# Kernel tuning notes

Measured on AMD Instinct MI355X. Metric: run time of the kernel, lower is better.

Reference implementation:

```python
import jax, jax.numpy as jnp
import numpy as np

N = 384          # residues / nodes
E = 12288        # edges (avg degree 32)
D_LM = 1024      # BERT hidden
D_NODE = 256     # extra node features -> D_LM + D_NODE = 1280
D = 1280         # node_emb_size
H = D // 10      # 128, dis/mask MLP hidden
M = 64           # masked positions


def setup_inputs() -> dict:
    key = jax.random.key(0)
    ks = jax.random.split(key, 16)
    s = lambda d_in: 1.0 / np.sqrt(d_in)
    inp = {
        "lm_embedding": jax.random.normal(ks[0], (1, N + 2, D_LM), jnp.float32),
        "node_feat": jax.random.normal(ks[1], (N, D_NODE), jnp.float32),
        # positive distances in [0.5, 1.5) so edge_weight = 1/(d^2+1e-6) is well scaled
        "edge_feat": jax.random.uniform(ks[2], (E, 1), jnp.float32) + 0.5,
        "src": jax.random.randint(ks[3], (E,), 0, N, jnp.int32),
        "dst": jax.random.randint(ks[4], (E,), 0, N, jnp.int32),
        "mask_index": jax.random.randint(ks[5], (M,), 0, N, jnp.int32),
        # GINConv apply-func linears (stored as [in, out]; torch Linear is x @ W.T + b)
        "W_gin0": jax.random.normal(ks[6], (D, D), jnp.float32) * s(D),
        "b_gin0": jnp.zeros((D,), jnp.float32),
        "W_gin1": jax.random.normal(ks[7], (D, D), jnp.float32) * s(D),
        "b_gin1": jnp.zeros((D,), jnp.float32),
        # dis_nn: Linear(D,H) -> ReLU -> Linear(H,30)
        "Wd1": jax.random.normal(ks[8], (D, H), jnp.float32) * s(D),
        "bd1": jnp.zeros((H,), jnp.float32),
        "Wd2": jax.random.normal(ks[9], (H, 30), jnp.float32) * s(H),
        "bd2": jnp.zeros((30,), jnp.float32),
        # mask_nn: Linear(D,H) -> ReLU -> Linear(H,2) -> Tanh
        "Wm1": jax.random.normal(ks[10], (D, H), jnp.float32) * s(D),
        "bm1": jnp.zeros((H,), jnp.float32),
        "Wm2": jax.random.normal(ks[11], (H, 2), jnp.float32) * s(H),
        "bm2": jnp.zeros((2,), jnp.float32),
    }
    return inp


def _gin(x, src, dst, edge_weight, W, b):
    # DGL GINConv (eps=0, 'sum'): Linear( x + sum_{e:(u->v)} w_e * x_u )
    msg = x[src] * edge_weight                      # [E, D] gather-multiply
    agg = jax.ops.segment_sum(msg, dst, num_segments=N)  # scatter-sum to dst
    return (x + agg) @ W + b


def reference(lm_embedding, node_feat, edge_feat, src, dst, mask_index,
              W_gin0, b_gin0, W_gin1, b_gin1,
              Wd1, bd1, Wd2, bd2, Wm1, bm1, Wm2, bm2):
    # node_feat0: strip CLS/SEP tokens, concat with node features -> [N, D]
    node_feat0 = jnp.concatenate([lm_embedding[0, 1:-1, :], node_feat], axis=1)
    edge_weight = 1.0 / (edge_feat ** 2 + 1e-6)     # [E, 1]

    # original uses node_feat0.data (detached) as GIN input
    x0 = jax.lax.stop_gradient(node_feat0)
    h = _gin(x0, src, dst, edge_weight, W_gin0, b_gin0)
    node_output = _gin(h, src, dst, edge_weight, W_gin1, b_gin1)
    node_output = node_output + node_feat0          # residual (use_lm=1)

    # pairwise squared differences: [N, N, D]
    dis_hid = (node_output[None, :, :] - node_output[:, None, :]) ** 2
    dh = dis_hid.reshape(-1, D)                     # [N*N, D]
    dis_pred = jax.nn.relu(dh @ Wd1 + bd1) @ Wd2 + bd2  # [N*N, 30]

    xm = node_output[mask_index]                    # [M, D]
    mask_pred = jnp.tanh(jax.nn.relu(xm @ Wm1 + bm1) @ Wm2 + bm2)  # [M, 2]
    return dis_pred, mask_pred
```

## Files before the change

### kernel.cpp

```cpp
#include <hip/hip_runtime.h>
#include <hip/hip_bf16.h>

#define NN 384
#define EE 12288
#define DD 1280
#define HH 128
#define DISROWS (NN*NN)

typedef short bf16x8 __attribute__((ext_vector_type(8)));
typedef short bf16x4 __attribute__((ext_vector_type(4)));
typedef float f32x4  __attribute__((ext_vector_type(4)));

__device__ __forceinline__ unsigned short f2bf(float x){
  unsigned u = __builtin_bit_cast(unsigned, x);
  u += 0x7fffu + ((u >> 16) & 1u);
  return (unsigned short)(u >> 16);
}
__device__ __forceinline__ float bf2f(unsigned short h){
  unsigned u = ((unsigned)h) << 16;
  return __builtin_bit_cast(float, u);
}
__device__ __forceinline__ short f2bf_fast(float x){
  return (short)__bfloat16_as_ushort(__float2bfloat16(x));
}
__device__ __forceinline__ void glds16(const short* g, short* l){
  __builtin_amdgcn_global_load_lds((const __attribute__((address_space(1))) void*)g,
                                   (__attribute__((address_space(3))) void*)l, 16, 0, 0);
}

__device__ __forceinline__ void tsplit_body(const float* __restrict__ W,
                                            short* __restrict__ Thi, short* __restrict__ Tlo,
                                            int R, int C, int bx, int by, int t,
                                            float* tile ){
  int rb = by*64, cb = bx*64;
  int r  = t >> 2;
  int cs = (t & 3) * 16;
  const float* sp = W + (long)(rb + r)*C + cb + cs;
  #pragma unroll
  for (int i = 0; i < 16; i += 4){
    f32x4 v = *(const f32x4*)(sp + i);
    tile[r*65 + cs+i+0] = v[0]; tile[r*65 + cs+i+1] = v[1];
    tile[r*65 + cs+i+2] = v[2]; tile[r*65 + cs+i+3] = v[3];
  }
  __syncthreads();
  int cp = t >> 2;
  int rs = (t & 3) * 16;
  bf16x8 vh0, vh1, vl0, vl1;
  #pragma unroll
  for (int i = 0; i < 8; ++i){
    float f = tile[(rs+i)*65 + cp];
    unsigned short h = f2bf(f);
    vh0[i] = (short)h; vl0[i] = (short)f2bf(f - bf2f(h));
  }
  #pragma unroll
  for (int i = 0; i < 8; ++i){
    float f = tile[(rs+8+i)*65 + cp];
    unsigned short h = f2bf(f);
    vh1[i] = (short)h; vl1[i] = (short)f2bf(f - bf2f(h));
  }
  long ob = (long)(cb + cp)*R + rb + rs;
  *(bf16x8*)&Thi[ob]   = vh0;
  *(bf16x8*)&Thi[ob+8] = vh1;
  if (Tlo){
    *(bf16x8*)&Tlo[ob]   = vl0;
    *(bf16x8*)&Tlo[ob+8] = vl1;
  }
}

__global__ void k_prep(const float* __restrict__ lm, const float* __restrict__ nf,
                       float* __restrict__ x0,
                       const int* __restrict__ dst, const float* __restrict__ ef,
                       int* __restrict__ offs, int* __restrict__ sorted,
                       float* __restrict__ ew,
                       const float* __restrict__ Wd1, short* __restrict__ W1t,
                       const float* __restrict__ Wd2, short* __restrict__ W2t,
                       const float* __restrict__ Wg0, short* __restrict__ WtAh,
                       short* __restrict__ WtAl){
  __shared__ __align__(16) float sh[64*65];
  const int b = blockIdx.x;
  const int t = threadIdx.x;
  if (b < 960){
    int i = b*512 + t;
    int n = i / 1280;
    int d = i - n*1280;
    x0[i] = (d < 1024) ? lm[(n+1)*1024 + d] : nf[n*256 + (d-1024)];
    return;
  }
  if (b == 960){
    int* cnt = (int*)sh;
    int* base = cnt + 512;
    if (t < 512) cnt[t] = 0;
    __syncthreads();
    for (int e = t; e < EE; e += 512){
      atomicAdd(&cnt[dst[e]], 1);
      float f = ef[e];
      ew[e] = 1.0f/(f*f + 1e-6f);
    }
    __syncthreads();
    for (int off = 1; off < 512; off <<= 1){
      int v = (t >= off) ? cnt[t - off] : 0;
      __syncthreads();
      cnt[t] += v;
      __syncthreads();
    }
    if (t < NN){
      int excl = t ? cnt[t-1] : 0;
      offs[t] = excl;
      base[t] = excl;
    }
    if (t == 0) offs[NN] = EE;
    __syncthreads();
    for (int e = t; e < EE; e += 512){
      int p = atomicAdd(&base[dst[e]], 1);
      sorted[p] = e;
    }
    return;
  }
  if (b < 1002){
    int g = b - 961;
    if (g < 40){
      if (t < 256) tsplit_body(Wd1, W1t, nullptr, DD, HH, g & 1, g >> 1, t, sh);
      else { __syncthreads(); }
      return;
    }
    for (int i = t; i < 32*HH; i += 512){
      int c = i >> 7, h = i & 127;
      float v = (c < 30) ? Wd2[h*30 + c] : 0.f;
      W2t[i] = (short)f2bf(v);
    }
    return;
  }
  {
    int g = b - 1002;
    if (t < 256) tsplit_body(Wg0, WtAh, WtAl, DD, DD, g % 20, g / 20, t, sh);
    else { __syncthreads(); }
  }
}

__global__ void k_agg(const float* __restrict__ X, const float* __restrict__ ew,
                      const int* __restrict__ src, const int* __restrict__ offs,
                      const int* __restrict__ sorted, float* __restrict__ Y){
  __shared__ int   s_off[160];
  __shared__ float s_w[160];
  const int v = blockIdx.x;
  const int d = blockIdx.y*256 + threadIdx.x;
  const int t = threadIdx.x;
  float acc = X[(long)v*DD + d];
  const int b = offs[v], e = offs[v+1];
  for (int c0 = b; c0 < e; c0 += 160){
    int n = e - c0; if (n > 160) n = 160;
    __syncthreads();
    if (t < n){
      int eid = sorted[c0 + t];
      s_off[t] = src[eid]*DD;
      s_w[t]   = ew[eid];
    }
    __syncthreads();
    int k = 0;
    for (; k + 4 <= n; k += 4){
      acc += s_w[k]  *X[s_off[k]   + d];
      acc += s_w[k+1]*X[s_off[k+1] + d];
      acc += s_w[k+2]*X[s_off[k+2] + d];
      acc += s_w[k+3]*X[s_off[k+3] + d];
    }
    for (; k < n; ++k) acc += s_w[k]*X[s_off[k] + d];
  }
  Y[(long)v*DD + d] = acc;
}

__launch_bounds__(256, 2)
__global__ void k_gin_gemm(const float* __restrict__ Y, const short* __restrict__ Whi,
                           const short* __restrict__ Wlo, float* __restrict__ P){
  __shared__ __align__(16) short Ahi[128*40], Alo[128*40], Bhi[128*40], Blo[128*40];
  const int m0 = blockIdx.x*128;
  const int n0 = blockIdx.y*128;
  const int kbase = blockIdx.z*320;
  const int t = threadIdx.x, w = t >> 6, lane = t & 63;
  const int l15 = lane & 15, l4 = lane >> 4;
  f32x4 acc[2][8];
  #pragma unroll
  for (int m = 0; m < 2; ++m)
    #pragma unroll
    for (int n = 0; n < 8; ++n) acc[m][n] = (f32x4){0.f,0.f,0.f,0.f};

  const int row = t >> 1, half = t & 1;
  const float* ap  = Y   + (long)(m0+row)*DD + half*16;
  const short* bph = Whi + (long)(n0+row)*DD + half*16;
  const short* bpl = Wlo + (long)(n0+row)*DD + half*16;

  for (int kk = 0; kk < 10; ++kk){
    int d0 = kbase + kk*32;
    __syncthreads();
    #pragma unroll
    for (int g = 0; g < 2; ++g){
      f32x4 v0 = *(const f32x4*)(ap + d0 + g*8);
      f32x4 v1 = *(const f32x4*)(ap + d0 + g*8 + 4);
      bf16x8 vh, vl;
      #pragma unroll
      for (int q = 0; q < 4; ++q){
        unsigned short h0 = f2bf(v0[q]);
        vh[q]   = (short)h0; vl[q]   = (short)f2bf(v0[q] - bf2f(h0));
        unsigned short h1 = f2bf(v1[q]);
        vh[4+q] = (short)h1; vl[4+q] = (short)f2bf(v1[q] - bf2f(h1));
      }
      *(bf16x8*)&Ahi[row*40 + half*16 + g*8] = vh;
      *(bf16x8*)&Alo[row*40 + half*16 + g*8] = vl;
    }
    *(bf16x8*)&Bhi[row*40 + half*16]     = *(const bf16x8*)(bph + d0);
    *(bf16x8*)&Bhi[row*40 + half*16 + 8] = *(const bf16x8*)(bph + d0 + 8);
    *(bf16x8*)&Blo[row*40 + half*16]     = *(const bf16x8*)(bpl + d0);
    *(bf16x8*)&Blo[row*40 + half*16 + 8] = *(const bf16x8*)(bpl + d0 + 8);
    __syncthreads();

    bf16x8 ah[2], al[2];
    #pragma unroll
    for (int m = 0; m < 2; ++m){
      int rr = w*32 + m*16 + l15;
      ah[m] = *(const bf16x8*)&Ahi[rr*40 + l4*8];
      al[m] = *(const bf16x8*)&Alo[rr*40 + l4*8];
    }
    #pragma unroll
    for (int n = 0; n < 8; ++n){
      int rr = n*16 + l15;
      bf16x8 bh = *(const bf16x8*)&Bhi[rr*40 + l4*8];
      bf16x8 bl = *(const bf16x8*)&Blo[rr*40 + l4*8];
      #pragma unroll
      for (int m = 0; m < 2; ++m){
        acc[m][n] = __builtin_amdgcn_mfma_f32_16x16x32_bf16(ah[m], bh, acc[m][n], 0,0,0);
        acc[m][n] = __builtin_amdgcn_mfma_f32_16x16x32_bf16(ah[m], bl, acc[m][n], 0,0,0);
        acc[m][n] = __builtin_amdgcn_mfma_f32_16x16x32_bf16(al[m], bh, acc[m][n], 0,0,0);
      }
    }
  }
  float* Pz = P + (long)blockIdx.z*NN*DD;
  #pragma unroll
  for (int m = 0; m < 2; ++m){
    #pragma unroll
    for (int n = 0; n < 8; ++n){
      int gr0 = m0 + w*32 + m*16 + l4*4;
      int gc  = n0 + n*16 + l15;
      #pragma unroll
      for (int r = 0; r < 4; ++r)
        Pz[(long)(gr0+r)*DD + gc] = acc[m][n][r];
    }
  }
}

__global__ void k_red_t(const float* __restrict__ P, const float* __restrict__ bias,
                        const float* __restrict__ resid, float* __restrict__ Out,
                        const float* __restrict__ Wg1, short* __restrict__ WtAh,
                        short* __restrict__ WtAl){
  __shared__ __align__(16) float sh[64*65];
  const int b = blockIdx.x;
  if (b >= 480){
    if (Wg1){
      int g = b - 480;
      tsplit_body(Wg1, WtAh, WtAl, DD, DD, g % 20, g / 20, threadIdx.x, sh);
    }
    return;
  }
  const int i = b*256 + threadIdx.x;
  const int col = (i*4) % DD;
  const f32x4* P4 = (const f32x4*)P;
  f32x4 s = P4[i];
  s += P4[i + 122880];
  s += P4[i + 2*122880];
  s += P4[i + 3*122880];
  s += *(const f32x4*)(bias + col);
  if (resid) s += ((const f32x4*)resid)[i];
  ((f32x4*)Out)[i] = s;
}

__launch_bounds__(256, 3)
__global__ void k_dis(const float* __restrict__ X, const short* __restrict__ W1t,
                      const float* __restrict__ bd1, const short* __restrict__ W2t,
                      const float* __restrict__ bd2, float* __restrict__ out,
                      const int* __restrict__ midx,
                      const float* __restrict__ Wm1, const float* __restrict__ bm1,
                      const float* __restrict__ Wm2, const float* __restrict__ bm2){
  __shared__ __align__(16) short smem[25088];
  const int b = blockIdx.x;
  const int t = threadIdx.x;

  if (b >= 600){
    float* tl = (float*)smem;
    int m = b - 600;
    if (t < HH){
      const float* x = X + (long)midx[m]*DD;
      float a0 = 0.f, a1 = 0.f, a2 = 0.f, a3 = 0.f;
      for (int d = 0; d < DD; d += 4){
        a0 += x[d]   * Wm1[(d)*HH + t];
        a1 += x[d+1] * Wm1[(d+1)*HH + t];
        a2 += x[d+2] * Wm1[(d+2)*HH + t];
        a3 += x[d+3] * Wm1[(d+3)*HH + t];
      }
      float v = a0 + a1 + a2 + a3 + bm1[t];
      tl[t] = v > 0.f ? v : 0.f;
    }
    __syncthreads();
    if (t < 2){
      float s = bm2[t];
      for (int h = 0; h < HH; ++h) s += tl[h]*Wm2[h*2 + t];
      out[(long)DISROWS*30 + m*2 + t] = tanhf(s);
    }
    return;
  }

  int k = 0, rem = b;
  while (rem >= 2*(24 - k)){ rem -= 2*(24 - k); ++k; }
  int ib = 2*k;
  if (rem >= 24 - k){ ++ib; rem -= 24 - k; }
  const int jb = k + rem;
  const int i0 = ib*8, j0 = jb*16;

  const int w = t >> 6, lane = t & 63;
  const int l15 = lane & 15, l4 = lane >> 4;

  short* WA = smem;
  float* XF = (float*)(smem + 16384);
  short* TL = smem;
  float* OT = (float*)(smem + 17408);

  f32x4 acc[2][8];
  #pragma unroll
  for (int m = 0; m < 2; ++m)
    #pragma unroll
    for (int n = 0; n < 8; ++n) acc[m][n] = (f32x4){0.f,0.f,0.f,0.f};

  const short* wsrc[4];
  #pragma unroll
  for (int i = 0; i < 4; ++i){
    int hb = w*32 + i*8 + (lane >> 3);
    wsrc[i] = W1t + (long)hb*DD + (((lane & 7) ^ (hb & 7))*8);
  }
  const float* xsrc[6];
  int xli[6];
  #pragma unroll
  for (int g = 0; g < 6; ++g){
    int idx = g*256 + t;
    int rowl = idx >> 6, col = idx & 63;
    int grow = (rowl < 8) ? (i0 + rowl) : (j0 + rowl - 8);
    xsrc[g] = X + (long)grow*DD + col;
    xli[g] = rowl*68 + col;
  }

  float xr[6];
  #pragma unroll
  for (int i = 0; i < 4; ++i)
    glds16(wsrc[i], WA + (w*32 + i*8)*64);
  #pragma unroll
  for (int g = 0; g < 6; ++g) xr[g] = xsrc[g][0];
  #pragma unroll
  for (int g = 0; g < 6; ++g) XF[xli[g]] = xr[g];
  __syncthreads();

  for (int mk = 0; mk < 20; ++mk){
    const int cb = mk & 1;
    short* WAc = WA + cb*8192;
    float* XFc = XF + cb*1632;
    short* WAn = WA + (cb^1)*8192;
    float* XFn = XF + (cb^1)*1632;
    if (mk < 19){
      #pragma unroll
      for (int i = 0; i < 4; ++i)
        glds16(wsrc[i] + (mk+1)*64, WAn + (w*32 + i*8)*64);
      #pragma unroll
      for (int g = 0; g < 6; ++g) xr[g] = xsrc[g][(mk+1)*64];
    }
    #pragma unroll
    for (int ks = 0; ks < 2; ++ks){
      f32x4 xj0 = *(const f32x4*)&XFc[(8 + l15)*68 + ks*32 + l4*8];
      f32x4 xj1 = *(const f32x4*)&XFc[(8 + l15)*68 + ks*32 + l4*8 + 4];
      bf16x8 a[2];
      #pragma unroll
      for (int m = 0; m < 2; ++m){
        const float* xip = &XFc[(2*w + m)*68 + ks*32 + l4*8];
        f32x4 xi0 = *(const f32x4*)xip;
        f32x4 xi1 = *(const f32x4*)(xip + 4);
        bf16x8 av;
        #pragma unroll
        for (int q = 0; q < 4; ++q){ float dl = xj0[q]-xi0[q]; av[q]   = f2bf_fast(dl*dl); }
        #pragma unroll
        for (int q = 0; q < 4; ++q){ float dl = xj1[q]-xi1[q]; av[4+q] = f2bf_fast(dl*dl); }
        a[m] = av;
      }
      #pragma unroll
      for (int n = 0; n < 8; ++n){
        bf16x8 wf = *(const bf16x8*)&WAc[(n*16 + l15)*64 + (((ks*4 + l4) ^ (l15 & 7))*8)];
        acc[0][n] = __builtin_amdgcn_mfma_f32_16x16x32_bf16(wf, a[0], acc[0][n], 0,0,0);
        acc[1][n] = __builtin_amdgcn_mfma_f32_16x16x32_bf16(wf, a[1], acc[1][n], 0,0,0);
      }
    }
    if (mk < 19){
      #pragma unroll
      for (int g = 0; g < 6; ++g) XFn[xli[g]] = xr[g];
    }
    __syncthreads();
  }

  f32x4 bd1v[8];
  #pragma unroll
  for (int n = 0; n < 8; ++n) bd1v[n] = *(const f32x4*)(bd1 + n*16 + l4*4);
  #pragma unroll
  for (int m = 0; m < 2; ++m){
    int pair = (2*w + m)*16 + l15;
    #pragma unroll
    for (int n = 0; n < 8; ++n){
      bf16x4 pv;
      #pragma unroll
      for (int r = 0; r < 4; ++r){
        float v = acc[m][n][r] + bd1v[n][r];
        v = v > 0.f ? v : 0.f;
        pv[r] = f2bf_fast(v);
      }
      *(bf16x4*)&TL[pair*136 + n*16 + l4*4] = pv;
    }
  }
  __syncthreads();

  f32x4 acc2[2][2];
  #pragma unroll
  for (int m2 = 0; m2 < 2; ++m2)
    #pragma unroll
    for (int nn = 0; nn < 2; ++nn) acc2[m2][nn] = (f32x4){0.f,0.f,0.f,0.f};
  #pragma unroll
  for (int hs = 0; hs < 4; ++hs){
    bf16x8 b2[2];
    #pragma unroll
    for (int nn = 0; nn < 2; ++nn)
      b2[nn] = *(const bf16x8*)&W2t[(nn*16 + l15)*HH + hs*32 + l4*8];
    #pragma unroll
    for (int m2 = 0; m2 < 2; ++m2){
      bf16x8 a2 = *(const bf16x8*)&TL[(w*32 + m2*16 + l15)*136 + hs*32 + l4*8];
      #pragma unroll
      for (int nn = 0; nn < 2; ++nn)
        acc2[m2][nn] = __builtin_amdgcn_mfma_f32_16x16x32_bf16(a2, b2[nn], acc2[m2][nn], 0,0,0);
    }
  }
  #pragma unroll
  for (int m2 = 0; m2 < 2; ++m2){
    #pragma unroll
    for (int nn = 0; nn < 2; ++nn){
      int cc = nn*16 + l15;
      if (cc < 30){
        float b2v = bd2[cc];
        #pragma unroll
        for (int r = 0; r < 4; ++r)
          OT[(w*32 + m2*16 + l4*4 + r)*30 + cc] = acc2[m2][nn][r] + b2v;
      }
    }
  }
  __syncthreads();

  {
    int i = t >> 5;
    int ca = (t & 31)*15;
    long nbase = ((long)(i0 + i)*NN + j0)*30 + ca;
    const float* nsrc = OT + i*480 + ca;
    #pragma unroll
    for (int q = 0; q < 15; ++q) out[nbase + q] = nsrc[q];
    int j = t >> 4;
    int s = t & 15;
    int ii = s >> 1;
    int c0 = (s & 1)*15;
    long mbase = ((long)(j0 + j)*NN + i0 + ii)*30 + c0;
    const float* msrc = OT + ii*480 + j*30 + c0;
    #pragma unroll
    for (int q = 0; q < 15; ++q) out[mbase + q] = msrc[q];
  }
}

extern "C" void kernel_launch(void* const* d_in, const int* in_sizes, int n_in,
                              void* d_out, int out_size, void* d_ws, size_t ws_size,
                              hipStream_t stream){
  const float* lm   = (const float*)d_in[0];
  const float* nf   = (const float*)d_in[1];
  const float* ef   = (const float*)d_in[2];
  const int*   src  = (const int*)d_in[3];
  const int*   dst  = (const int*)d_in[4];
  const int*   midx = (const int*)d_in[5];
  const float* Wg0  = (const float*)d_in[6];
  const float* bg0  = (const float*)d_in[7];
  const float* Wg1  = (const float*)d_in[8];
  const float* bg1  = (const float*)d_in[9];
  const float* Wd1  = (const float*)d_in[10];
  const float* bd1  = (const float*)d_in[11];
  const float* Wd2  = (const float*)d_in[12];
  const float* bd2  = (const float*)d_in[13];
  const float* Wm1  = (const float*)d_in[14];
  const float* bm1  = (const float*)d_in[15];
  const float* Wm2  = (const float*)d_in[16];
  const float* bm2  = (const float*)d_in[17];
  float* dis = (float*)d_out;

  char* ws = (char*)d_ws;
  size_t off = 0;
  auto alloc = [&](size_t bytes)->void*{
    void* p = ws + off; off += (bytes + 255) & ~(size_t)255; return p;
  };
  float* x0   = (float*)alloc((size_t)NN*DD*4);
  float* yb   = (float*)alloc((size_t)NN*DD*4);
  float* hb   = (float*)alloc((size_t)NN*DD*4);
  float* ew   = (float*)alloc((size_t)EE*4);
  int*   offs = (int*)alloc((NN+1)*4);
  int*   sorted = (int*)alloc(EE*4);
  short* WtAh = (short*)alloc((size_t)DD*DD*2);
  short* WtAl = (short*)alloc((size_t)DD*DD*2);
  short* W1t  = (short*)alloc((size_t)HH*DD*2);
  short* W2t  = (short*)alloc((size_t)32*HH*2);
  float* P    = (float*)alloc((size_t)4*NN*DD*4);

  k_prep<<<1402,512,0,stream>>>(lm, nf, x0, dst, ef, offs, sorted, ew,
                                Wd1, W1t, Wd2, W2t, Wg0, WtAh, WtAl);

  k_agg<<<dim3(384,5),256,0,stream>>>(x0, ew, src, offs, sorted, yb);
  k_gin_gemm<<<dim3(3,10,4),256,0,stream>>>(yb, WtAh, WtAl, P);
  k_red_t<<<880,256,0,stream>>>(P, bg0, nullptr, hb, Wg1, WtAh, WtAl);

  k_agg<<<dim3(384,5),256,0,stream>>>(hb, ew, src, offs, sorted, yb);
  k_gin_gemm<<<dim3(3,10,4),256,0,stream>>>(yb, WtAh, WtAl, P);
  k_red_t<<<480,256,0,stream>>>(P, bg1, x0, hb, nullptr, nullptr, nullptr);

  k_dis<<<664,256,0,stream>>>(hb, W1t, bd1, W2t, bd2, dis,
                              midx, Wm1, bm1, Wm2, bm2);
}
```

Before: 142.3 us.

## Retile dis-MLP GEMM into 4x4 warp tiles with register-held xi rows

The pairwise-difference GEMM loop is restructured. Each warp now covers 4 i-rows by 64 hidden units instead of 2 i-rows by all 128, and the K step drops from 64 to 32, giving 40 iterations. The xi rows are loaded directly from global memory into registers and only the xj rows are staged in LDS, which shrinks shared memory use and LDS reads per MFMA. In exchange there are twice as many barriers, more per-thread global loads, and higher register pressure from the 4x4 accumulator tile.

New measurement: 159.7 us. +12.2%, slower.

```diff
diff --git a/kernel.cpp b/kernel.cpp
--- a/kernel.cpp
+++ b/kernel.cpp
@@ -10,6 +10,7 @@
 typedef short bf16x8 __attribute__((ext_vector_type(8)));
 typedef short bf16x4 __attribute__((ext_vector_type(4)));
 typedef float f32x4  __attribute__((ext_vector_type(4)));
+typedef float f32x2  __attribute__((ext_vector_type(2)));
 
 __device__ __forceinline__ unsigned short f2bf(float x){
   unsigned u = __builtin_bit_cast(unsigned, x);
@@ -315,97 +316,94 @@
 
   const int w = t >> 6, lane = t & 63;
   const int l15 = lane & 15, l4 = lane >> 4;
+  const int wi = w & 1, wh = w >> 1;
 
   short* WA = smem;
-  float* XF = (float*)(smem + 16384);
+  float* XJ = (float*)(smem + 8192);
   short* TL = smem;
   float* OT = (float*)(smem + 17408);
 
-  f32x4 acc[2][8];
-  #pragma unroll
-  for (int m = 0; m < 2; ++m)
-    #pragma unroll
-    for (int n = 0; n < 8; ++n) acc[m][n] = (f32x4){0.f,0.f,0.f,0.f};
-
-  const short* wsrc[4];
-  #pragma unroll
-  for (int i = 0; i < 4; ++i){
-    int hb = w*32 + i*8 + (lane >> 3);
-    wsrc[i] = W1t + (long)hb*DD + (((lane & 7) ^ (hb & 7))*8);
-  }
-  const float* xsrc[6];
-  int xli[6];
-  #pragma unroll
-  for (int g = 0; g < 6; ++g){
-    int idx = g*256 + t;
-    int rowl = idx >> 6, col = idx & 63;
-    int grow = (rowl < 8) ? (i0 + rowl) : (j0 + rowl - 8);
-    xsrc[g] = X + (long)grow*DD + col;
-    xli[g] = rowl*68 + col;
-  }
-
-  float xr[6];
-  #pragma unroll
-  for (int i = 0; i < 4; ++i)
-    glds16(wsrc[i], WA + (w*32 + i*8)*64);
-  #pragma unroll
-  for (int g = 0; g < 6; ++g) xr[g] = xsrc[g][0];
-  #pragma unroll
-  for (int g = 0; g < 6; ++g) XF[xli[g]] = xr[g];
+  f32x4 acc[4][4];
+  #pragma unroll
+  for (int m = 0; m < 4; ++m)
+    #pragma unroll
+    for (int n = 0; n < 4; ++n) acc[m][n] = (f32x4){0.f,0.f,0.f,0.f};
+
+  const short* wsrc[2]; int wdst[2];
+  #pragma unroll
+  for (int i = 0; i < 2; ++i){
+    int h = (w*2 + i)*16 + (lane >> 2);
+    int s = lane & 3;
+    wsrc[i] = W1t + (long)h*DD + ((s ^ ((h >> 1) & 3))*8);
+    wdst[i] = (w*2 + i)*512;
+  }
+  const float* xjsrc = X + (long)(j0 + (t >> 4))*DD + (t & 15)*2;
+  const int xjli = (t >> 4)*36 + (t & 15)*2;
+  const float* xip[4];
+  #pragma unroll
+  for (int m = 0; m < 4; ++m)
+    xip[m] = X + (long)(i0 + wi*4 + m)*DD + l4*8;
+
+  glds16(wsrc[0], WA + wdst[0]);
+  glds16(wsrc[1], WA + wdst[1]);
+  { f32x2 v = *(const f32x2*)xjsrc; *(f32x2*)&XJ[xjli] = v; }
+  f32x4 xa[4], xb[4];
+  #pragma unroll
+  for (int m = 0; m < 4; ++m){
+    xa[m] = *(const f32x4*)xip[m];
+    xb[m] = *(const f32x4*)(xip[m] + 4);
+  }
   __syncthreads();
 
-  for (int mk = 0; mk < 20; ++mk){
-    const int cb = mk & 1;
-    short* WAc = WA + cb*8192;
-    float* XFc = XF + cb*1632;
-    short* WAn = WA + (cb^1)*8192;
-    float* XFn = XF + (cb^1)*1632;
-    if (mk < 19){
-      #pragma unroll
-      for (int i = 0; i < 4; ++i)
-        glds16(wsrc[i] + (mk+1)*64, WAn + (w*32 + i*8)*64);
-      #pragma unroll
-      for (int g = 0; g < 6; ++g) xr[g] = xsrc[g][(mk+1)*64];
-    }
-    #pragma unroll
-    for (int ks = 0; ks < 2; ++ks){
-      f32x4 xj0 = *(const f32x4*)&XFc[(8 + l15)*68 + ks*32 + l4*8];
-      f32x4 xj1 = *(const f32x4*)&XFc[(8 + l15)*68 + ks*32 + l4*8 + 4];
-      bf16x8 a[2];
-      #pragma unroll
-      for (int m = 0; m < 2; ++m){
-        const float* xip = &XFc[(2*w + m)*68 + ks*32 + l4*8];
-        f32x4 xi0 = *(const f32x4*)xip;
-        f32x4 xi1 = *(const f32x4*)(xip + 4);
-        bf16x8 av;
-        #pragma unroll
-        for (int q = 0; q < 4; ++q){ float dl = xj0[q]-xi0[q]; av[q]   = f2bf_fast(dl*dl); }
-        #pragma unroll
-        for (int q = 0; q < 4; ++q){ float dl = xj1[q]-xi1[q]; av[4+q] = f2bf_fast(dl*dl); }
-        a[m] = av;
+  const int wro = (l4 ^ ((l15 >> 1) & 3))*8;
+  for (int mk = 0; mk < 40; ++mk){
+    const int cur = mk & 1, nxt = cur ^ 1;
+    const int d1 = (mk+1)*32;
+    if (mk < 39){
+      glds16(wsrc[0] + d1, WA + nxt*4096 + wdst[0]);
+      glds16(wsrc[1] + d1, WA + nxt*4096 + wdst[1]);
+    }
+    const float* XJc = XJ + cur*576;
+    f32x4 xj0 = *(const f32x4*)&XJc[l15*36 + l4*8];
+    f32x4 xj1 = *(const f32x4*)&XJc[l15*36 + l4*8 + 4];
+    bf16x8 a[4];
+    #pragma unroll
+    for (int m = 0; m < 4; ++m){
+      bf16x8 av;
+      #pragma unroll
+      for (int q = 0; q < 4; ++q){ float d = xj0[q]-xa[m][q]; av[q]   = f2bf_fast(d*d); }
+      #pragma unroll
+      for (int q = 0; q < 4; ++q){ float d = xj1[q]-xb[m][q]; av[4+q] = f2bf_fast(d*d); }
+      a[m] = av;
+    }
+    if (mk < 39){
+      #pragma unroll
+      for (int m = 0; m < 4; ++m){
+        xa[m] = *(const f32x4*)(xip[m] + d1);
+        xb[m] = *(const f32x4*)(xip[m] + d1 + 4);
       }
-      #pragma unroll
-      for (int n = 0; n < 8; ++n){
-        bf16x8 wf = *(const bf16x8*)&WAc[(n*16 + l15)*64 + (((ks*4 + l4) ^ (l15 & 7))*8)];
-        acc[0][n] = __builtin_amdgcn_mfma_f32_16x16x32_bf16(wf, a[0], acc[0][n], 0,0,0);
-        acc[1][n] = __builtin_amdgcn_mfma_f32_16x16x32_bf16(wf, a[1], acc[1][n], 0,0,0);
-      }
-    }
-    if (mk < 19){
-      #pragma unroll
-      for (int g = 0; g < 6; ++g) XFn[xli[g]] = xr[g];
-    }
-    __syncthreads();
-  }
-
-  f32x4 bd1v[8];
-  #pragma unroll
-  for (int n = 0; n < 8; ++n) bd1v[n] = *(const f32x4*)(bd1 + n*16 + l4*4);
-  #pragma unroll
-  for (int m = 0; m < 2; ++m){
-    int pair = (2*w + m)*16 + l15;
-    #pragma unroll
-    for (int n = 0; n < 8; ++n){
+      f32x2 xjn = *(const f32x2*)(xjsrc + d1);
+      *(f32x2*)&XJ[nxt*576 + xjli] = xjn;
+    }
+    const short* WAc = WA + cur*4096;
+    #pragma unroll
+    for (int n = 0; n < 4; ++n){
+      bf16x8 wf = *(const bf16x8*)&WAc[((wh*4 + n)*16 + l15)*32 + wro];
+      #pragma unroll
+      for (int m = 0; m < 4; ++m)
+        acc[m][n] = __builtin_amdgcn_mfma_f32_16x16x32_bf16(wf, a[m], acc[m][n], 0,0,0);
+    }
+    __syncthreads();
+  }
+
+  f32x4 bd1v[4];
+  #pragma unroll
+  for (int n = 0; n < 4; ++n) bd1v[n] = *(const f32x4*)(bd1 + wh*64 + n*16 + l4*4);
+  #pragma unroll
+  for (int m = 0; m < 4; ++m){
+    int pair = (wi*4 + m)*16 + l15;
+    #pragma unroll
+    for (int n = 0; n < 4; ++n){
       bf16x4 pv;
       #pragma unroll
       for (int r = 0; r < 4; ++r){
@@ -413,7 +411,7 @@
         v = v > 0.f ? v : 0.f;
         pv[r] = f2bf_fast(v);
       }
-      *(bf16x4*)&TL[pair*136 + n*16 + l4*4] = pv;
+      *(bf16x4*)&TL[pair*136 + wh*64 + n*16 + l4*4] = pv;
     }
   }
   __syncthreads();
```

## Fuse GIN prep, aggregation, GEMM and reduce into one persistent kernel with grid barriers

Applied to the files above, without the earlier changes.

Replaces the seven launches for prep, two aggregations, two split-bf16 GEMMs and two reductions with a single persistent 256-block kernel whose stages are separated by a software grid barrier. The edge sort becomes a global atomic count, a scan in block 0 and a parallel placement step. Both GIN weight matrices are now split and transposed up front into separate buffers. GEMM tiles shrink to 128x64 with one 16-row slab per wave. The aim is to remove launch gaps and tail effects between small stages. In exchange it adds barrier spin cost, relies on all 256 blocks being co-resident, and may lose per-stage parallelism.

New measurement: 336.7 us. +136.6%, slower.

```diff
diff --git a/kernel.cpp b/kernel.cpp
--- a/kernel.cpp
+++ b/kernel.cpp
@@ -28,247 +28,257 @@
                                    (__attribute__((address_space(3))) void*)l, 16, 0, 0);
 }
 
-__device__ __forceinline__ void tsplit_body(const float* __restrict__ W,
-                                            short* __restrict__ Thi, short* __restrict__ Tlo,
-                                            int R, int C, int bx, int by, int t,
-                                            float* tile ){
+__device__ __forceinline__ void gridbar(int* ibar){
+  __syncthreads();
+  if (threadIdx.x == 0){
+    __threadfence();
+    int g = atomicAdd(&ibar[1], 0);
+    int v = atomicAdd(&ibar[0], 1);
+    if (v == 255){
+      atomicExch(&ibar[0], 0);
+      atomicAdd(&ibar[1], 1);
+    } else {
+      int iters = 0;
+      while (atomicAdd(&ibar[1], 0) == g && iters < (1<<20)){
+        ++iters;
+        __builtin_amdgcn_s_sleep(8);
+      }
+    }
+    __threadfence();
+  }
+  __syncthreads();
+}
+
+__device__ __forceinline__ void tsplit512(const float* __restrict__ W,
+                                          short* __restrict__ Thi, short* __restrict__ Tlo,
+                                          int R, int C, int bx, int by, int t, float* tile){
   int rb = by*64, cb = bx*64;
-  int r  = t >> 2;
-  int cs = (t & 3) * 16;
+  int r = t >> 3, cs = (t & 7)*8;
   const float* sp = W + (long)(rb + r)*C + cb + cs;
-  #pragma unroll
-  for (int i = 0; i < 16; i += 4){
-    f32x4 v = *(const f32x4*)(sp + i);
-    tile[r*65 + cs+i+0] = v[0]; tile[r*65 + cs+i+1] = v[1];
-    tile[r*65 + cs+i+2] = v[2]; tile[r*65 + cs+i+3] = v[3];
-  }
+  f32x4 v0 = *(const f32x4*)sp;
+  f32x4 v1 = *(const f32x4*)(sp + 4);
+  tile[r*65 + cs+0] = v0[0]; tile[r*65 + cs+1] = v0[1];
+  tile[r*65 + cs+2] = v0[2]; tile[r*65 + cs+3] = v0[3];
+  tile[r*65 + cs+4] = v1[0]; tile[r*65 + cs+5] = v1[1];
+  tile[r*65 + cs+6] = v1[2]; tile[r*65 + cs+7] = v1[3];
   __syncthreads();
-  int cp = t >> 2;
-  int rs = (t & 3) * 16;
-  bf16x8 vh0, vh1, vl0, vl1;
+  int cp = t >> 3, rs = (t & 7)*8;
+  bf16x8 vh, vl;
   #pragma unroll
   for (int i = 0; i < 8; ++i){
     float f = tile[(rs+i)*65 + cp];
     unsigned short h = f2bf(f);
-    vh0[i] = (short)h; vl0[i] = (short)f2bf(f - bf2f(h));
-  }
-  #pragma unroll
-  for (int i = 0; i < 8; ++i){
-    float f = tile[(rs+8+i)*65 + cp];
-    unsigned short h = f2bf(f);
-    vh1[i] = (short)h; vl1[i] = (short)f2bf(f - bf2f(h));
+    vh[i] = (short)h; vl[i] = (short)f2bf(f - bf2f(h));
   }
   long ob = (long)(cb + cp)*R + rb + rs;
-  *(bf16x8*)&Thi[ob]   = vh0;
-  *(bf16x8*)&Thi[ob+8] = vh1;
-  if (Tlo){
-    *(bf16x8*)&Tlo[ob]   = vl0;
-    *(bf16x8*)&Tlo[ob+8] = vl1;
-  }
-}
-
-__global__ void k_prep(const float* __restrict__ lm, const float* __restrict__ nf,
-                       float* __restrict__ x0,
-                       const int* __restrict__ dst, const float* __restrict__ ef,
-                       int* __restrict__ offs, int* __restrict__ sorted,
-                       float* __restrict__ ew,
-                       const float* __restrict__ Wd1, short* __restrict__ W1t,
-                       const float* __restrict__ Wd2, short* __restrict__ W2t,
-                       const float* __restrict__ Wg0, short* __restrict__ WtAh,
-                       short* __restrict__ WtAl){
-  __shared__ __align__(16) float sh[64*65];
-  const int b = blockIdx.x;
-  const int t = threadIdx.x;
-  if (b < 960){
-    int i = b*512 + t;
-    int n = i / 1280;
-    int d = i - n*1280;
-    x0[i] = (d < 1024) ? lm[(n+1)*1024 + d] : nf[n*256 + (d-1024)];
-    return;
-  }
-  if (b == 960){
-    int* cnt = (int*)sh;
-    int* base = cnt + 512;
-    if (t < 512) cnt[t] = 0;
+  *(bf16x8*)&Thi[ob] = vh;
+  if (Tlo) *(bf16x8*)&Tlo[ob] = vl;
+}
+
+__device__ void agg_stage(const float* __restrict__ X, float* __restrict__ Y,
+                          const float* __restrict__ ew, const int* __restrict__ src_,
+                          const int* __restrict__ offs, const int* __restrict__ sorted,
+                          int b, int t, char* sm){
+  int*   s_off = (int*)sm;
+  float* s_w   = (float*)(sm + 2048);
+  for (int u = b; u < 768; u += 256){
+    int v = u >> 1;
+    int dh = (u & 1)*640;
+    int d0 = dh + t;
+    int d1 = dh + 512 + t;
+    float a0 = X[(long)v*DD + d0];
+    float a1 = (t < 128) ? X[(long)v*DD + d1] : 0.f;
+    const int eb = offs[v], ee = offs[v+1];
+    for (int c0 = eb; c0 < ee; c0 += 512){
+      int n = ee - c0; if (n > 512) n = 512;
+      __syncthreads();
+      if (t < n){
+        int eid = sorted[c0 + t];
+        s_off[t] = src_[eid]*DD;
+        s_w[t]   = ew[eid];
+      }
+      __syncthreads();
+      int k = 0;
+      for (; k + 4 <= n; k += 4){
+        a0 += s_w[k]*X[s_off[k]+d0];   a0 += s_w[k+1]*X[s_off[k+1]+d0];
+        a0 += s_w[k+2]*X[s_off[k+2]+d0]; a0 += s_w[k+3]*X[s_off[k+3]+d0];
+        if (t < 128){
+          a1 += s_w[k]*X[s_off[k]+d1];   a1 += s_w[k+1]*X[s_off[k+1]+d1];
+          a1 += s_w[k+2]*X[s_off[k+2]+d1]; a1 += s_w[k+3]*X[s_off[k+3]+d1];
+        }
+      }
+      for (; k < n; ++k){
+        a0 += s_w[k]*X[s_off[k]+d0];
+        if (t < 128) a1 += s_w[k]*X[s_off[k]+d1];
+      }
+    }
+    Y[(long)v*DD + d0] = a0;
+    if (t < 128) Y[(long)v*DD + d1] = a1;
     __syncthreads();
-    for (int e = t; e < EE; e += 512){
-      atomicAdd(&cnt[dst[e]], 1);
-      float f = ef[e];
-      ew[e] = 1.0f/(f*f + 1e-6f);
-    }
+  }
+}
+
+__device__ void gemm_stage(const float* __restrict__ Y, const short* __restrict__ Whi,
+                           const short* __restrict__ Wlo, float* __restrict__ P,
+                           int b, int t, char* sm){
+  if (b < 240){
+    short* Ahi = (short*)sm;
+    short* Alo = Ahi + 5120;
+    short* Bhi = Alo + 5120;
+    short* Blo = Bhi + 2560;
+    const int z = b / 60, rest = b % 60;
+    const int m0 = (rest % 3)*128, n0 = (rest / 3)*64;
+    const int kbase = z*320;
+    const int w = t >> 6, lane = t & 63, l15 = lane & 15, l4 = lane >> 4;
+    f32x4 acc[4];
+    #pragma unroll
+    for (int n = 0; n < 4; ++n) acc[n] = (f32x4){0.f,0.f,0.f,0.f};
+    const int arow = t >> 2, aq = t & 3;
+    const float* ap = Y + (long)(m0 + arow)*DD + aq*8;
+    for (int kk = 0; kk < 10; ++kk){
+      const int d0 = kbase + kk*32;
+      __syncthreads();
+      {
+        f32x4 v0 = *(const f32x4*)(ap + d0);
+        f32x4 v1 = *(const f32x4*)(ap + d0 + 4);
+        bf16x8 vh, vl;
+        #pragma unroll
+        for (int q = 0; q < 4; ++q){
+          unsigned short h0 = f2bf(v0[q]);
+          vh[q]   = (short)h0; vl[q]   = (short)f2bf(v0[q] - bf2f(h0));
+          unsigned short h1 = f2bf(v1[q]);
+          vh[4+q] = (short)h1; vl[4+q] = (short)f2bf(v1[q] - bf2f(h1));
+        }
+        *(bf16x8*)&Ahi[arow*40 + aq*8] = vh;
+        *(bf16x8*)&Alo[arow*40 + aq*8] = vl;
+      }
+      if (t < 256){
+        const short* bph = Whi + (long)(n0 + (t>>2))*DD + (t&3)*8 + d0;
+        const short* bpl = Wlo + (long)(n0 + (t>>2))*DD + (t&3)*8 + d0;
+        *(bf16x8*)&Bhi[(t>>2)*40 + (t&3)*8] = *(const bf16x8*)bph;
+        *(bf16x8*)&Blo[(t>>2)*40 + (t&3)*8] = *(const bf16x8*)bpl;
+      }
+      __syncthreads();
+      bf16x8 ah = *(const bf16x8*)&Ahi[(w*16 + l15)*40 + l4*8];
+      bf16x8 al = *(const bf16x8*)&Alo[(w*16 + l15)*40 + l4*8];
+      #pragma unroll
+      for (int n = 0; n < 4; ++n){
+        bf16x8 bh = *(const bf16x8*)&Bhi[(n*16 + l15)*40 + l4*8];
+        bf16x8 bl = *(const bf16x8*)&Blo[(n*16 + l15)*40 + l4*8];
+        acc[n] = __builtin_amdgcn_mfma_f32_16x16x32_bf16(ah, bh, acc[n], 0,0,0);
+        acc[n] = __builtin_amdgcn_mfma_f32_16x16x32_bf16(ah, bl, acc[n], 0,0,0);
+        acc[n] = __builtin_amdgcn_mfma_f32_16x16x32_bf16(al, bh, acc[n], 0,0,0);
+      }
+    }
+    float* Pz = P + (long)z*NN*DD;
+    #pragma unroll
+    for (int n = 0; n < 4; ++n){
+      int gc = n0 + n*16 + l15;
+      #pragma unroll
+      for (int r = 0; r < 4; ++r)
+        Pz[(long)(m0 + w*16 + l4*4 + r)*DD + gc] = acc[n][r];
+    }
+  }
+}
+
+__device__ void red_stage(const float* __restrict__ P, const float* __restrict__ bias,
+                          const float* __restrict__ resid, float* __restrict__ Out,
+                          int b, int t){
+  if (t < 480){
+    const int i = b*480 + t;
+    const int col = (i*4) % DD;
+    const f32x4* P4 = (const f32x4*)P;
+    f32x4 s = P4[i];
+    s += P4[i + 122880];
+    s += P4[i + 2*122880];
+    s += P4[i + 3*122880];
+    s += *(const f32x4*)(bias + col);
+    if (resid) s += ((const f32x4*)resid)[i];
+    ((f32x4*)Out)[i] = s;
+  }
+}
+
+__global__ __launch_bounds__(512, 4)
+void k_chain(const float* __restrict__ lm, const float* __restrict__ nf,
+             const int* __restrict__ dst_, const float* __restrict__ ef,
+             const int* __restrict__ src_,
+             const float* __restrict__ Wg0, const float* __restrict__ Wg1,
+             const float* __restrict__ Wd1, const float* __restrict__ Wd2,
+             const float* __restrict__ bg0, const float* __restrict__ bg1,
+             int* ibar, int* gcnt, int* offs, int* basep, int* sorted,
+             float* ew, float* x0, float* yb, float* hb,
+             short* WtAh, short* WtAl, short* WtBh, short* WtBl,
+             short* W1t, short* W2t, float* P){
+  __shared__ __align__(16) char sm[40960];
+  const int b = blockIdx.x, t = threadIdx.x;
+
+  if (t < 480){
+    int i = (b*480 + t)*4;
+    int n = i / 1280, d = i - n*1280;
+    f32x4 v;
+    if (d < 1024) v = *(const f32x4*)&lm[(n+1)*1024 + d];
+    else          v = *(const f32x4*)&nf[n*256 + (d-1024)];
+    *(f32x4*)&x0[i] = v;
+  }
+  if (t < 48){
+    int e = b*48 + t;
+    float f = ef[e];
+    ew[e] = 1.0f/(f*f + 1e-6f);
+    atomicAdd(&gcnt[dst_[e]], 1);
+  }
+  {
+    float* tile = (float*)sm;
+    for (int u = b; u < 841; u += 256){
+      __syncthreads();
+      if (u < 400)       tsplit512(Wg0, WtAh, WtAl, DD, DD, u % 20, u / 20, t, tile);
+      else if (u < 800){ int g = u - 400; tsplit512(Wg1, WtBh, WtBl, DD, DD, g % 20, g / 20, t, tile); }
+      else if (u < 840){ int g = u - 800; tsplit512(Wd1, W1t, nullptr, DD, HH, g & 1, g >> 1, t, tile); }
+      else {
+        for (int i = t; i < 32*HH; i += 512){
+          int c = i >> 7, h = i & 127;
+          float v = (c < 30) ? Wd2[h*30 + c] : 0.f;
+          W2t[i] = (short)f2bf(v);
+        }
+      }
+    }
+  }
+  gridbar(ibar);
+  if (b == 0){
+    int* s = (int*)sm;
+    int c = (t < NN) ? gcnt[t] : 0;
+    s[t] = c;
     __syncthreads();
     for (int off = 1; off < 512; off <<= 1){
-      int v = (t >= off) ? cnt[t - off] : 0;
-      __syncthreads();
-      cnt[t] += v;
+      int v = (t >= off) ? s[t-off] : 0;
+      __syncthreads();
+      s[t] += v;
       __syncthreads();
     }
     if (t < NN){
-      int excl = t ? cnt[t-1] : 0;
+      int excl = s[t] - c;
       offs[t] = excl;
-      base[t] = excl;
+      basep[t] = excl;
     }
     if (t == 0) offs[NN] = EE;
-    __syncthreads();
-    for (int e = t; e < EE; e += 512){
-      int p = atomicAdd(&base[dst[e]], 1);
-      sorted[p] = e;
-    }
-    return;
-  }
-  if (b < 1002){
-    int g = b - 961;
-    if (g < 40){
-      if (t < 256) tsplit_body(Wd1, W1t, nullptr, DD, HH, g & 1, g >> 1, t, sh);
-      else { __syncthreads(); }
-      return;
-    }
-    for (int i = t; i < 32*HH; i += 512){
-      int c = i >> 7, h = i & 127;
-      float v = (c < 30) ? Wd2[h*30 + c] : 0.f;
-      W2t[i] = (short)f2bf(v);
-    }
-    return;
-  }
-  {
-    int g = b - 1002;
-    if (t < 256) tsplit_body(Wg0, WtAh, WtAl, DD, DD, g % 20, g / 20, t, sh);
-    else { __syncthreads(); }
-  }
-}
-
-__global__ void k_agg(const float* __restrict__ X, const float* __restrict__ ew,
-                      const int* __restrict__ src, const int* __restrict__ offs,
-                      const int* __restrict__ sorted, float* __restrict__ Y){
-  __shared__ int   s_off[160];
-  __shared__ float s_w[160];
-  const int v = blockIdx.x;
-  const int d = blockIdx.y*256 + threadIdx.x;
-  const int t = threadIdx.x;
-  float acc = X[(long)v*DD + d];
-  const int b = offs[v], e = offs[v+1];
-  for (int c0 = b; c0 < e; c0 += 160){
-    int n = e - c0; if (n > 160) n = 160;
-    __syncthreads();
-    if (t < n){
-      int eid = sorted[c0 + t];
-      s_off[t] = src[eid]*DD;
-      s_w[t]   = ew[eid];
-    }
-    __syncthreads();
-    int k = 0;
-    for (; k + 4 <= n; k += 4){
-      acc += s_w[k]  *X[s_off[k]   + d];
-      acc += s_w[k+1]*X[s_off[k+1] + d];
-      acc += s_w[k+2]*X[s_off[k+2] + d];
-      acc += s_w[k+3]*X[s_off[k+3] + d];
-    }
-    for (; k < n; ++k) acc += s_w[k]*X[s_off[k] + d];
-  }
-  Y[(long)v*DD + d] = acc;
-}
-
-__launch_bounds__(256, 2)
-__global__ void k_gin_gemm(const float* __restrict__ Y, const short* __restrict__ Whi,
-                           const short* __restrict__ Wlo, float* __restrict__ P){
-  __shared__ __align__(16) short Ahi[128*40], Alo[128*40], Bhi[128*40], Blo[128*40];
-  const int m0 = blockIdx.x*128;
-  const int n0 = blockIdx.y*128;
-  const int kbase = blockIdx.z*320;
-  const int t = threadIdx.x, w = t >> 6, lane = t & 63;
-  const int l15 = lane & 15, l4 = lane >> 4;
-  f32x4 acc[2][8];
-  #pragma unroll
-  for (int m = 0; m < 2; ++m)
-    #pragma unroll
-    for (int n = 0; n < 8; ++n) acc[m][n] = (f32x4){0.f,0.f,0.f,0.f};
-
-  const int row = t >> 1, half = t & 1;
-  const float* ap  = Y   + (long)(m0+row)*DD + half*16;
-  const short* bph = Whi + (long)(n0+row)*DD + half*16;
-  const short* bpl = Wlo + (long)(n0+row)*DD + half*16;
-
-  for (int kk = 0; kk < 10; ++kk){
-    int d0 = kbase + kk*32;
-    __syncthreads();
-    #pragma unroll
-    for (int g = 0; g < 2; ++g){
-      f32x4 v0 = *(const f32x4*)(ap + d0 + g*8);
-      f32x4 v1 = *(const f32x4*)(ap + d0 + g*8 + 4);
-      bf16x8 vh, vl;
-      #pragma unroll
-      for (int q = 0; q < 4; ++q){
-        unsigned short h0 = f2bf(v0[q]);
-        vh[q]   = (short)h0; vl[q]   = (short)f2bf(v0[q] - bf2f(h0));
-        unsigned short h1 = f2bf(v1[q]);
-        vh[4+q] = (short)h1; vl[4+q] = (short)f2bf(v1[q] - bf2f(h1));
-      }
-      *(bf16x8*)&Ahi[row*40 + half*16 + g*8] = vh;
-      *(bf16x8*)&Alo[row*40 + half*16 + g*8] = vl;
-    }
-    *(bf16x8*)&Bhi[row*40 + half*16]     = *(const bf16x8*)(bph + d0);
-    *(bf16x8*)&Bhi[row*40 + half*16 + 8] = *(const bf16x8*)(bph + d0 + 8);
-    *(bf16x8*)&Blo[row*40 + half*16]     = *(const bf16x8*)(bpl + d0);
-    *(bf16x8*)&Blo[row*40 + half*16 + 8] = *(const bf16x8*)(bpl + d0 + 8);
-    __syncthreads();
-
-    bf16x8 ah[2], al[2];
-    #pragma unroll
-    for (int m = 0; m < 2; ++m){
-      int rr = w*32 + m*16 + l15;
-      ah[m] = *(const bf16x8*)&Ahi[rr*40 + l4*8];
-      al[m] = *(const bf16x8*)&Alo[rr*40 + l4*8];
-    }
-    #pragma unroll
-    for (int n = 0; n < 8; ++n){
-      int rr = n*16 + l15;
-      bf16x8 bh = *(const bf16x8*)&Bhi[rr*40 + l4*8];
-      bf16x8 bl = *(const bf16x8*)&Blo[rr*40 + l4*8];
-      #pragma unroll
-      for (int m = 0; m < 2; ++m){
-        acc[m][n] = __builtin_amdgcn_mfma_f32_16x16x32_bf16(ah[m], bh, acc[m][n], 0,0,0);
-        acc[m][n] = __builtin_amdgcn_mfma_f32_16x16x32_bf16(ah[m], bl, acc[m][n], 0,0,0);
-        acc[m][n] = __builtin_amdgcn_mfma_f32_16x16x32_bf16(al[m], bh, acc[m][n], 0,0,0);
-      }
-    }
-  }
-  float* Pz = P + (long)blockIdx.z*NN*DD;
-  #pragma unroll
-  for (int m = 0; m < 2; ++m){
-    #pragma unroll
-    for (int n = 0; n < 8; ++n){
-      int gr0 = m0 + w*32 + m*16 + l4*4;
-      int gc  = n0 + n*16 + l15;
-      #pragma unroll
-      for (int r = 0; r < 4; ++r)
-        Pz[(long)(gr0+r)*DD + gc] = acc[m][n][r];
-    }
-  }
-}
-
-__global__ void k_red_t(const float* __restrict__ P, const float* __restrict__ bias,
-                        const float* __restrict__ resid, float* __restrict__ Out,
-                        const float* __restrict__ Wg1, short* __restrict__ WtAh,
-                        short* __restrict__ WtAl){
-  __shared__ __align__(16) float sh[64*65];
-  const int b = blockIdx.x;
-  if (b >= 480){
-    if (Wg1){
-      int g = b - 480;
-      tsplit_body(Wg1, WtAh, WtAl, DD, DD, g % 20, g / 20, threadIdx.x, sh);
-    }
-    return;
-  }
-  const int i = b*256 + threadIdx.x;
-  const int col = (i*4) % DD;
-  const f32x4* P4 = (const f32x4*)P;
-  f32x4 s = P4[i];
-  s += P4[i + 122880];
-  s += P4[i + 2*122880];
-  s += P4[i + 3*122880];
-  s += *(const f32x4*)(bias + col);
-  if (resid) s += ((const f32x4*)resid)[i];
-  ((f32x4*)Out)[i] = s;
+  }
+  gridbar(ibar);
+  if (t < 48){
+    int e = b*48 + t;
+    int p = atomicAdd(&basep[dst_[e]], 1);
+    sorted[p] = e;
+  }
+  gridbar(ibar);
+  agg_stage(x0, yb, ew, src_, offs, sorted, b, t, sm);
+  gridbar(ibar);
+  gemm_stage(yb, WtAh, WtAl, P, b, t, sm);
+  gridbar(ibar);
+  red_stage(P, bg0, nullptr, hb, b, t);
+  gridbar(ibar);
+  agg_stage(hb, yb, ew, src_, offs, sorted, b, t, sm);
+  gridbar(ibar);
+  gemm_stage(yb, WtBh, WtBl, P, b, t, sm);
+  gridbar(ibar);
+  red_stage(P, bg1, x0, hb, b, t);
 }
 
 __launch_bounds__(256, 3)
@@ -498,29 +508,29 @@
   auto alloc = [&](size_t bytes)->void*{
     void* p = ws + off; off += (bytes + 255) & ~(size_t)255; return p;
   };
-  float* x0   = (float*)alloc((size_t)NN*DD*4);
-  float* yb   = (float*)alloc((size_t)NN*DD*4);
-  float* hb   = (float*)alloc((size_t)NN*DD*4);
-  float* ew   = (float*)alloc((size_t)EE*4);
-  int*   offs = (int*)alloc((NN+1)*4);
+  int*   ibar   = (int*)alloc(4096);
+  int*   gcnt   = ibar + 16;
+  int*   offs   = (int*)alloc((NN+1)*4);
+  int*   basep  = (int*)alloc(NN*4);
   int*   sorted = (int*)alloc(EE*4);
-  short* WtAh = (short*)alloc((size_t)DD*DD*2);
-  short* WtAl = (short*)alloc((size_t)DD*DD*2);
-  short* W1t  = (short*)alloc((size_t)HH*DD*2);
-  short* W2t  = (short*)alloc((size_t)32*HH*2);
-  float* P    = (float*)alloc((size_t)4*NN*DD*4);
-
-  k_prep<<<1402,512,0,stream>>>(lm, nf, x0, dst, ef, offs, sorted, ew,
-                                Wd1, W1t, Wd2, W2t, Wg0, WtAh, WtAl);
-
-  k_agg<<<dim3(384,5),256,0,stream>>>(x0, ew, src, offs, sorted, yb);
-  k_gin_gemm<<<dim3(3,10,4),256,0,stream>>>(yb, WtAh, WtAl, P);
-  k_red_t<<<880,256,0,stream>>>(P, bg0, nullptr, hb, Wg1, WtAh, WtAl);
-
-  k_agg<<<dim3(384,5),256,0,stream>>>(hb, ew, src, offs, sorted, yb);
-  k_gin_gemm<<<dim3(3,10,4),256,0,stream>>>(yb, WtAh, WtAl, P);
-  k_red_t<<<480,256,0,stream>>>(P, bg1, x0, hb, nullptr, nullptr, nullptr);
-
-  k_dis<<<664,256,0,stream>>>(hb, W1t, bd1, W2t, bd2, dis,
-                              midx, Wm1, bm1, Wm2, bm2);
-}
+  float* ew     = (float*)alloc((size_t)EE*4);
+  float* x0     = (float*)alloc((size_t)NN*DD*4);
+  float* yb     = (float*)alloc((size_t)NN*DD*4);
+  float* hb     = (float*)alloc((size_t)NN*DD*4);
+  short* WtAh   = (short*)alloc((size_t)DD*DD*2);
+  short* WtAl   = (short*)alloc((size_t)DD*DD*2);
+  short* WtBh   = (short*)alloc((size_t)DD*DD*2);
+  short* WtBl   = (short*)alloc((size_t)DD*DD*2);
+  short* W1t    = (short*)alloc((size_t)HH*DD*2);
+  short* W2t    = (short*)alloc((size_t)32*HH*2);
+  float* P      = (float*)alloc((size_t)4*NN*DD*4);
+
+  hipMemsetAsync(ibar, 0, 4096, stream);
+  k_chain<<<256, 512, 0, stream>>>(lm, nf, dst, ef, src,
+                                   Wg0, Wg1, Wd1, Wd2, bg0, bg1,
+                                   ibar, gcnt, offs, basep, sorted,
+                                   ew, x0, yb, hb,
+                                   WtAh, WtAl, WtBh, WtBl, W1t, W2t, P);
+  k_dis<<<664, 256, 0, stream>>>(hb, W1t, bd1, W2t, bd2, dis,
+                                 midx, Wm1, bm1, Wm2, bm2);
+}
```

## Emit bf16 hi/lo split from aggregation and double GIN GEMM split-K

Applied to the files above, without the earlier changes.

The aggregation kernel now writes the bf16 hi/lo split of its fp32 output directly, so the GIN GEMM loads pre-split bf16 tiles instead of converting fp32 per tile. Split-K is raised from 4 to 8, giving 240 blocks instead of 120 for better CU occupancy, and the reduction kernel sums 8 partial buffers. The partial buffer doubles in size, which adds reduction traffic. The dis kernel's squared-difference computation is also rewritten in vector form.

Result: faster. 121.5 us (-14.6%).

```diff
diff --git a/kernel.cpp b/kernel.cpp
--- a/kernel.cpp
+++ b/kernel.cpp
@@ -139,7 +139,8 @@
 
 __global__ void k_agg(const float* __restrict__ X, const float* __restrict__ ew,
                       const int* __restrict__ src, const int* __restrict__ offs,
-                      const int* __restrict__ sorted, float* __restrict__ Y){
+                      const int* __restrict__ sorted,
+                      short* __restrict__ Yh, short* __restrict__ Yl){
   __shared__ int   s_off[160];
   __shared__ float s_w[160];
   const int v = blockIdx.x;
@@ -165,16 +166,19 @@
     }
     for (; k < n; ++k) acc += s_w[k]*X[s_off[k] + d];
   }
-  Y[(long)v*DD + d] = acc;
+  unsigned short h = f2bf(acc);
+  Yh[(long)v*DD + d] = (short)h;
+  Yl[(long)v*DD + d] = (short)f2bf(acc - bf2f(h));
 }
 
 __launch_bounds__(256, 2)
-__global__ void k_gin_gemm(const float* __restrict__ Y, const short* __restrict__ Whi,
-                           const short* __restrict__ Wlo, float* __restrict__ P){
+__global__ void k_gin_gemm(const short* __restrict__ Yh, const short* __restrict__ Yl,
+                           const short* __restrict__ Whi, const short* __restrict__ Wlo,
+                           float* __restrict__ P){
   __shared__ __align__(16) short Ahi[128*40], Alo[128*40], Bhi[128*40], Blo[128*40];
   const int m0 = blockIdx.x*128;
   const int n0 = blockIdx.y*128;
-  const int kbase = blockIdx.z*320;
+  const int kbase = blockIdx.z*160;
   const int t = threadIdx.x, w = t >> 6, lane = t & 63;
   const int l15 = lane & 15, l4 = lane >> 4;
   f32x4 acc[2][8];
@@ -184,28 +188,18 @@
     for (int n = 0; n < 8; ++n) acc[m][n] = (f32x4){0.f,0.f,0.f,0.f};
 
   const int row = t >> 1, half = t & 1;
-  const float* ap  = Y   + (long)(m0+row)*DD + half*16;
+  const short* aph = Yh  + (long)(m0+row)*DD + half*16;
+  const short* apl = Yl  + (long)(m0+row)*DD + half*16;
   const short* bph = Whi + (long)(n0+row)*DD + half*16;
   const short* bpl = Wlo + (long)(n0+row)*DD + half*16;
 
-  for (int kk = 0; kk < 10; ++kk){
+  for (int kk = 0; kk < 5; ++kk){
     int d0 = kbase + kk*32;
     __syncthreads();
-    #pragma unroll
-    for (int g = 0; g < 2; ++g){
-      f32x4 v0 = *(const f32x4*)(ap + d0 + g*8);
-      f32x4 v1 = *(const f32x4*)(ap + d0 + g*8 + 4);
-      bf16x8 vh, vl;
-      #pragma unroll
-      for (int q = 0; q < 4; ++q){
-        unsigned short h0 = f2bf(v0[q]);
-        vh[q]   = (short)h0; vl[q]   = (short)f2bf(v0[q] - bf2f(h0));
-        unsigned short h1 = f2bf(v1[q]);
-        vh[4+q] = (short)h1; vl[4+q] = (short)f2bf(v1[q] - bf2f(h1));
-      }
-      *(bf16x8*)&Ahi[row*40 + half*16 + g*8] = vh;
-      *(bf16x8*)&Alo[row*40 + half*16 + g*8] = vl;
-    }
+    *(bf16x8*)&Ahi[row*40 + half*16]     = *(const bf16x8*)(aph + d0);
+    *(bf16x8*)&Ahi[row*40 + half*16 + 8] = *(const bf16x8*)(aph + d0 + 8);
+    *(bf16x8*)&Alo[row*40 + half*16]     = *(const bf16x8*)(apl + d0);
+    *(bf16x8*)&Alo[row*40 + half*16 + 8] = *(const bf16x8*)(apl + d0 + 8);
     *(bf16x8*)&Bhi[row*40 + half*16]     = *(const bf16x8*)(bph + d0);
     *(bf16x8*)&Bhi[row*40 + half*16 + 8] = *(const bf16x8*)(bph + d0 + 8);
     *(bf16x8*)&Blo[row*40 + half*16]     = *(const bf16x8*)(bpl + d0);
@@ -263,9 +257,8 @@
   const int col = (i*4) % DD;
   const f32x4* P4 = (const f32x4*)P;
   f32x4 s = P4[i];
-  s += P4[i + 122880];
-  s += P4[i + 2*122880];
-  s += P4[i + 3*122880];
+  #pragma unroll
+  for (int z = 1; z < 8; ++z) s += P4[i + z*122880];
   s += *(const f32x4*)(bias + col);
   if (resid) s += ((const f32x4*)resid)[i];
   ((f32x4*)Out)[i] = s;
@@ -377,11 +370,14 @@
         const float* xip = &XFc[(2*w + m)*68 + ks*32 + l4*8];
         f32x4 xi0 = *(const f32x4*)xip;
         f32x4 xi1 = *(const f32x4*)(xip + 4);
+        f32x4 d0 = xj0 - xi0; d0 = d0*d0;
+        f32x4 d1 = xj1 - xi1; d1 = d1*d1;
         bf16x8 av;
         #pragma unroll
-        for (int q = 0; q < 4; ++q){ float dl = xj0[q]-xi0[q]; av[q]   = f2bf_fast(dl*dl); }
-        #pragma unroll
-        for (int q = 0; q < 4; ++q){ float dl = xj1[q]-xi1[q]; av[4+q] = f2bf_fast(dl*dl); }
+        for (int q = 0; q < 4; ++q){
+          av[q]   = f2bf_fast(d0[q]);
+          av[4+q] = f2bf_fast(d1[q]);
+        }
         a[m] = av;
       }
       #pragma unroll
@@ -499,8 +495,9 @@
     void* p = ws + off; off += (bytes + 255) & ~(size_t)255; return p;
   };
   float* x0   = (float*)alloc((size_t)NN*DD*4);
-  float* yb   = (float*)alloc((size_t)NN*DD*4);
   float* hb   = (float*)alloc((size_t)NN*DD*4);
+  short* Yh   = (short*)alloc((size_t)NN*DD*2);
+  short* Yl   = (short*)alloc((size_t)NN*DD*2);
   float* ew   = (float*)alloc((size_t)EE*4);
   int*   offs = (int*)alloc((NN+1)*4);
   int*   sorted = (int*)alloc(EE*4);
@@ -508,17 +505,17 @@
   short* WtAl = (short*)alloc((size_t)DD*DD*2);
   short* W1t  = (short*)alloc((size_t)HH*DD*2);
   short* W2t  = (short*)alloc((size_t)32*HH*2);
-  float* P    = (float*)alloc((size_t)4*NN*DD*4);
+  float* P    = (float*)alloc((size_t)8*NN*DD*4);
 
   k_prep<<<1402,512,0,stream>>>(lm, nf, x0, dst, ef, offs, sorted, ew,
                                 Wd1, W1t, Wd2, W2t, Wg0, WtAh, WtAl);
 
-  k_agg<<<dim3(384,5),256,0,stream>>>(x0, ew, src, offs, sorted, yb);
-  k_gin_gemm<<<dim3(3,10,4),256,0,stream>>>(yb, WtAh, WtAl, P);
+  k_agg<<<dim3(384,5),256,0,stream>>>(x0, ew, src, offs, sorted, Yh, Yl);
+  k_gin_gemm<<<dim3(3,10,8),256,0,stream>>>(Yh, Yl, WtAh, WtAl, P);
   k_red_t<<<880,256,0,stream>>>(P, bg0, nullptr, hb, Wg1, WtAh, WtAl);
 
-  k_agg<<<dim3(384,5),256,0,stream>>>(hb, ew, src, offs, sorted, yb);
-  k_gin_gemm<<<dim3(3,10,4),256,0,stream>>>(yb, WtAh, WtAl, P);
+  k_agg<<<dim3(384,5),256,0,stream>>>(hb, ew, src, offs, sorted, Yh, Yl);
+  k_gin_gemm<<<dim3(3,10,8),256,0,stream>>>(Yh, Yl, WtAh, WtAl, P);
   k_red_t<<<480,256,0,stream>>>(P, bg1, x0, hb, nullptr, nullptr, nullptr);
 
   k_dis<<<664,256,0,stream>>>(hb, W1t, bd1, W2t, bd2, dis,
```
